# Kernel optimization log

Measured on AMD Instinct MI355X. Metric: run time of the kernel, lower is better.

Reference implementation:

```python
import jax, jax.numpy as jnp
import numpy as np

PC_RANGE = (-51.2, -51.2, -5.0, 51.2, 51.2, 3.0)
IMG_H, IMG_W = 256.0, 704.0
EPS = 1e-5


def conv2d(x, w, b, pad):
    y = jax.lax.conv_general_dilated(x, w, (1, 1), ((pad, pad), (pad, pad)),
                                     dimension_numbers=('NCHW', 'OIHW', 'NCHW'))
    return y + b[None, :, None, None]


def bilinear_sample(feat, grid):
    # torch.F.grid_sample, bilinear, zeros padding, align_corners=False
    # feat (BN,C,H,W), grid (BN,Q,D,2) in [-1,1] -> (BN,C,Q,D)
    BN, C, H, W = feat.shape
    ix = (grid[..., 0] + 1.0) * (W * 0.5) - 0.5
    iy = (grid[..., 1] + 1.0) * (H * 0.5) - 0.5
    x0 = jnp.floor(ix); y0 = jnp.floor(iy)
    x1 = x0 + 1.0; y1 = y0 + 1.0
    wx1 = ix - x0; wx0 = 1.0 - wx1
    wy1 = iy - y0; wy0 = 1.0 - wy1

    def corner(f, xi, yi):
        inb = ((xi >= 0) & (xi < W) & (yi >= 0) & (yi < H)).astype(f.dtype)
        xc = jnp.clip(xi, 0, W - 1).astype(jnp.int32)
        yc = jnp.clip(yi, 0, H - 1).astype(jnp.int32)
        idx = (yc * W + xc).reshape(-1)
        v = f.reshape(C, H * W)[:, idx].reshape((C,) + xi.shape)
        return v * inb[None]

    def sample_one(f, x0b, y0b, x1b, y1b, w00, w01, w10, w11):
        return (corner(f, x0b, y0b) * w00[None] + corner(f, x1b, y0b) * w01[None]
                + corner(f, x0b, y1b) * w10[None] + corner(f, x1b, y1b) * w11[None])

    return jax.vmap(sample_one)(feat, x0, y0, x1, y1,
                                wx0 * wy0, wx1 * wy0, wx0 * wy1, wx1 * wy1)


def ihr_forward(feat, bev_queries, bev_pos, reference_points, lidar2img, img_aug,
                w_pos, b_pos, w_attn, b_attn, w_out, b_out,
                conv_w, conv_b, bn_gamma, bn_beta, bn_mean, bn_var,
                se_w, se_b, cbam_w, cbam_b, bev_h, bev_w):
    B, Q, C = bev_queries.shape
    N = lidar2img.shape[1]
    q = bev_queries + bev_pos
    off = q @ w_pos + b_pos                                   # (B,Q,1) height offset
    # only_use_height: z <- sigmoid(inverse_sigmoid(z) + off)
    z = jnp.clip(reference_points[..., 2:3], 0.0, 1.0)
    z = jnp.log(jnp.clip(z, EPS, None) / jnp.clip(1.0 - z, EPS, None))
    z = jax.nn.sigmoid(z + off[:, None])                      # (B,D,Q,1)
    rp = jnp.concatenate([reference_points[..., :2], z], -1)  # updated ref points

    # --- feature_sampling ---
    xyz = jnp.stack([
        rp[..., 0] * (PC_RANGE[3] - PC_RANGE[0]) + PC_RANGE[0],
        rp[..., 1] * (PC_RANGE[4] - PC_RANGE[1]) + PC_RANGE[1],
        rp[..., 2] * (PC_RANGE[5] - PC_RANGE[2]) + PC_RANGE[2]], -1)  # (B,D,Q,3)
    pts = jnp.concatenate([xyz, jnp.ones_like(xyz[..., :1])], -1)
    pts = jnp.transpose(pts, (1, 0, 2, 3))                    # (D,B,Q,4)
    D = pts.shape[0]
    cam = jnp.einsum('bnij,dbqj->dbnqi', lidar2img, pts)       # (D,B,N,Q,3)
    depth = cam[..., 2:3]
    mask = depth > EPS
    cam4 = jnp.concatenate([cam[..., :2] / jnp.maximum(depth, EPS), depth,
                            jnp.ones_like(depth)], -1)
    cam2 = jnp.einsum('bnij,dbnqj->dbnqi', img_aug, cam4)[..., :2]
    cam2 = cam2 / jnp.array([IMG_W, IMG_H], cam2.dtype)
    cam2 = (cam2 - 0.5) * 2.0
    mask = (mask & (cam2[..., 0:1] > -1.0) & (cam2[..., 0:1] < 1.0)
            & (cam2[..., 1:2] > -1.0) & (cam2[..., 1:2] < 1.0))
    bev_mask = jnp.nan_to_num(jnp.transpose(mask, (1, 4, 3, 2, 0)).astype(feat.dtype))  # (B,1,Q,N,D)
    grid = jnp.transpose(cam2, (1, 2, 3, 0, 4)).reshape(B * N, Q, D, 2)
    samp = bilinear_sample(feat, grid)                         # (BN,C,Q,D)
    samp = samp.reshape(B, N, C, Q, D).transpose(0, 2, 3, 1, 4)  # (B,C,Q,N,D)
    samp = jnp.nan_to_num(samp)

    attn = jax.nn.sigmoid(q @ w_attn + b_attn).reshape(B, 1, Q, N, 1) * bev_mask
    out = (samp * attn).sum(axis=(3, 4))                       # (B,C,Q)  (D==1)
    out = out.transpose(0, 2, 1) @ w_out + b_out + bev_queries  # (B,Q,C)

    # --- vtransform: Conv3x3 -> BN(eval) -> ReLU -> SE -> CBAM(spatial) ---
    x = out.transpose(0, 2, 1).reshape(B, C, bev_h, bev_w)
    x = conv2d(x, conv_w, conv_b, 1)
    inv = jax.lax.rsqrt(bn_var + 1e-5)
    x = bn_gamma[None, :, None, None] * (x - bn_mean[None, :, None, None]) * inv[None, :, None, None] + bn_beta[None, :, None, None]
    x = jax.nn.relu(x)
    s = jax.nn.sigmoid(x.mean(axis=(2, 3)) @ se_w + se_b)      # SE: GAP + 1x1 conv
    x = x * s[:, :, None, None]
    mx = x.max(axis=1, keepdims=True)
    av = x.mean(axis=1, keepdims=True)
    a = jax.nn.sigmoid(conv2d(jnp.concatenate([mx, av], 1), cbam_w, cbam_b, 3))
    x = x * a
    out = x.reshape(B, C, bev_h * bev_w).transpose(0, 2, 1)
    return out, rp


def setup_inputs() -> dict:
    key = jax.random.key(0)
    ks = jax.random.split(key, 16)
    B, N, C, Q, D = 1, 6, 256, 128 * 128, 1
    H, W = 32, 88
    return {
        'feat': jax.random.normal(ks[0], (B * N, C, H, W), jnp.float32),
        'bev_queries': jax.random.normal(ks[1], (B, Q, C), jnp.float32),
        'bev_pos': jax.random.normal(ks[2], (B, Q, C), jnp.float32),
        'reference_points': jax.random.uniform(ks[3], (B, D, Q, 3), jnp.float32),
        'lidar2img': jax.random.normal(ks[4], (B, N, 3, 4), jnp.float32),
        'img_aug': jax.random.normal(ks[5], (B, N, 3, 4), jnp.float32),
        'w_pos': jax.random.normal(ks[6], (C, 1), jnp.float32) * 0.02,
        'b_pos': jnp.zeros((1,), jnp.float32),
        'w_attn': jax.random.normal(ks[7], (C, N), jnp.float32) * 0.02,
        'b_attn': jnp.zeros((N,), jnp.float32),
        'w_out': jax.random.normal(ks[8], (C, C), jnp.float32) * 0.02,
        'b_out': jnp.zeros((C,), jnp.float32),
        'conv_w': jax.random.normal(ks[9], (C, C, 3, 3), jnp.float32) * 0.02,
        'conv_b': jnp.zeros((C,), jnp.float32),
        'bn_gamma': jnp.ones((C,), jnp.float32),
        'bn_beta': jnp.zeros((C,), jnp.float32),
        'bn_mean': jnp.zeros((C,), jnp.float32),
        'bn_var': jax.random.uniform(ks[10], (C,), jnp.float32, 0.5, 1.5),
        'se_w': jax.random.normal(ks[11], (C, C), jnp.float32) * 0.02,
        'se_b': jnp.zeros((C,), jnp.float32),
        'cbam_w': jax.random.normal(ks[12], (1, 2, 7, 7), jnp.float32) * 0.1,
        'cbam_b': jnp.zeros((1,), jnp.float32),
        'bev_h': 128,
        'bev_w': 128,
    }


def reference(feat, bev_queries, bev_pos, reference_points, lidar2img, img_aug,
              w_pos, b_pos, w_attn, b_attn, w_out, b_out,
              conv_w, conv_b, bn_gamma, bn_beta, bn_mean, bn_var,
              se_w, se_b, cbam_w, cbam_b, bev_h, bev_w):
    return ihr_forward(feat, bev_queries, bev_pos, reference_points, lidar2img, img_aug,
                       w_pos, b_pos, w_attn, b_attn, w_out, b_out,
                       conv_w, conv_b, bn_gamma, bn_beta, bn_mean, bn_var,
                       se_w, se_b, cbam_w, cbam_b, bev_h, bev_w)
```

## Files before the change

kernel.cpp:

```cpp
#include <hip/hip_runtime.h>

typedef float  f32x4 __attribute__((ext_vector_type(4)));
typedef short  s16x8 __attribute__((ext_vector_type(8)));
typedef short  s16x4 __attribute__((ext_vector_type(4)));

__device__ __forceinline__ float bf2f(short h) {
    union { unsigned u; float f; } v; v.u = ((unsigned)(unsigned short)h) << 16; return v.f;
}
__device__ __forceinline__ short f2bf(float f) {
    union { float f; unsigned u; } v; v.f = f;
    unsigned r = v.u + 0x7FFFu + ((v.u >> 16) & 1u);
    return (short)(r >> 16);
}
__device__ __forceinline__ float sigf(float x) { return 1.f / (1.f + __expf(-x)); }

__device__ __forceinline__ void gll16(const void* g, void* l) {
    __builtin_amdgcn_global_load_lds(
        (const __attribute__((address_space(1))) unsigned int*)(uintptr_t)g,
        (__attribute__((address_space(3))) unsigned int*)(uintptr_t)l,
        16, 0, 0);
}


__global__ __launch_bounds__(256) void k_prep(
    const float* __restrict__ feat, const float* __restrict__ w_out,
    const float* __restrict__ conv_w, short* __restrict__ featT,
    short* __restrict__ woT, short* __restrict__ w9,
    short* __restrict__ Xp, float* __restrict__ chan_sums)
{
    __shared__ float tile[64][65];
    int b = blockIdx.x, t = threadIdx.x;
    if (b < 2340) {
        ((f32x4*)Xp)[b * 256 + t] = (f32x4){0.f, 0.f, 0.f, 0.f};
    } else if (b < 3396) {
        int bb = b - 2340;
        int n = bb / 176, r = bb % 176, ct = r / 44, ht = r % 44;
        int ty = t >> 6, tx = t & 63;
        const float* src = feat + (n * 256 + ct * 64) * 2816 + ht * 64;
        #pragma unroll
        for (int i = 0; i < 16; ++i) {
            int cl = ty * 16 + i;
            tile[cl][tx] = src[cl * 2816 + tx];
        }
        __syncthreads();
        short* dst = featT + (n * 2816 + ht * 64) * 256 + ct * 64;
        #pragma unroll
        for (int i = 0; i < 16; ++i) {
            int row = ty * 16 + i;
            dst[row * 256 + tx] = f2bf(tile[tx][row]);
        }
    } else if (b < 3652) {
        int idx = (b - 3396) * 256 + t;
        int j = idx >> 8, c = idx & 255;
        woT[j * 256 + c] = f2bf(w_out[c * 256 + j]);
    } else if (b < 3908) {
        int oc = (b - 3652) * 256 + t;
        const float* src = conv_w + oc * 9;
        #pragma unroll
        for (int k = 0; k < 9; ++k) w9[k * 65536 + oc] = f2bf(src[k]);
    } else {
        if (t < 256) chan_sums[t] = 0.f;
    }
}

__global__ __launch_bounds__(256) void k_sample(
    const float* __restrict__ bev_q, const float* __restrict__ bev_pos,
    const float* __restrict__ refp, const float* __restrict__ l2i,
    const float* __restrict__ aug, const float* __restrict__ w_pos,
    const float* __restrict__ b_pos, const float* __restrict__ w_attn,
    const float* __restrict__ b_attn, const short* __restrict__ featT,
    short* __restrict__ S, float* __restrict__ rp_out)
{
    int lane = threadIdx.x & 63;
    int qi = blockIdx.x * 4 + (threadIdx.x >> 6);

    f32x4 qv = *(const f32x4*)(bev_q + qi * 256 + lane * 4);
    {
        f32x4 pv = *(const f32x4*)(bev_pos + qi * 256 + lane * 4);
        qv[0] += pv[0]; qv[1] += pv[1]; qv[2] += pv[2]; qv[3] += pv[3];
    }
    f32x4 wp = *(const f32x4*)(w_pos + lane * 4);
    float op = qv[0]*wp[0] + qv[1]*wp[1] + qv[2]*wp[2] + qv[3]*wp[3];

    float la[6] = {0.f,0.f,0.f,0.f,0.f,0.f};
    const float* wa = w_attn + lane * 24;
    #pragma unroll
    for (int i = 0; i < 4; ++i) {
        #pragma unroll
        for (int n = 0; n < 6; ++n) la[n] += qv[i] * wa[i * 6 + n];
    }
    #pragma unroll
    for (int m = 1; m < 64; m <<= 1) {
        op += __shfl_xor(op, m);
        #pragma unroll
        for (int n = 0; n < 6; ++n) la[n] += __shfl_xor(la[n], m);
    }
    float off = op + b_pos[0];
    float attn[6];
    #pragma unroll
    for (int n = 0; n < 6; ++n) attn[n] = sigf(la[n] + b_attn[n]);

    float rx = refp[qi * 3 + 0], ry = refp[qi * 3 + 1], rz = refp[qi * 3 + 2];
    float zc = fminf(fmaxf(rz, 0.f), 1.f);
    float lg = logf(fmaxf(zc, 1e-5f) / fmaxf(1.f - zc, 1e-5f));
    float zn = sigf(lg + off);
    if (lane == 0) {
        rp_out[qi * 3 + 0] = rx;
        rp_out[qi * 3 + 1] = ry;
        rp_out[qi * 3 + 2] = zn;
    }

    float X = rx * 102.4f - 51.2f;
    float Yc = ry * 102.4f - 51.2f;
    float Z = zn * 8.f - 5.f;

    f32x4 acc = {0.f, 0.f, 0.f, 0.f};
    auto corner = [&](int n, int xi, int yi, float w) {
        if (xi >= 0 && xi < 88 && yi >= 0 && yi < 32) {
            s16x4 v = *(const s16x4*)(featT + (((n * 32 + yi) * 88 + xi) << 8) + (lane << 2));
            acc[0] += w * bf2f(v[0]); acc[1] += w * bf2f(v[1]);
            acc[2] += w * bf2f(v[2]); acc[3] += w * bf2f(v[3]);
        }
    };
    for (int n = 0; n < 6; ++n) {
        const float* L = l2i + n * 12;
        float cx = L[0]*X + L[1]*Yc + L[2]*Z  + L[3];
        float cy = L[4]*X + L[5]*Yc + L[6]*Z  + L[7];
        float d  = L[8]*X + L[9]*Yc + L[10]*Z + L[11];
        float dd = fmaxf(d, 1e-5f);
        float ux = cx / dd, uy = cy / dd;
        const float* A = aug + n * 12;
        float ax = A[0]*ux + A[1]*uy + A[2]*d + A[3];
        float ay = A[4]*ux + A[5]*uy + A[6]*d + A[7];
        float gx = (ax * (1.f / 704.f) - 0.5f) * 2.f;
        float gy = (ay * (1.f / 256.f) - 0.5f) * 2.f;
        bool m = (d > 1e-5f) && (gx > -1.f) && (gx < 1.f) && (gy > -1.f) && (gy < 1.f);
        if (m) {
            float ix = (gx + 1.f) * 44.f - 0.5f;
            float iy = (gy + 1.f) * 16.f - 0.5f;
            float x0f = floorf(ix), y0f = floorf(iy);
            float wx1 = ix - x0f, wx0 = 1.f - wx1;
            float wy1 = iy - y0f, wy0 = 1.f - wy1;
            int x0 = (int)x0f, y0 = (int)y0f, x1 = x0 + 1, y1 = y0 + 1;
            float wn = attn[n];
            corner(n, x0, y0, wn * wx0 * wy0);
            corner(n, x1, y0, wn * wx1 * wy0);
            corner(n, x0, y1, wn * wx0 * wy1);
            corner(n, x1, y1, wn * wx1 * wy1);
        }
    }
    s16x4 sv;
    sv[0] = f2bf(acc[0]); sv[1] = f2bf(acc[1]);
    sv[2] = f2bf(acc[2]); sv[3] = f2bf(acc[3]);
    *(s16x4*)(S + qi * 256 + lane * 4) = sv;
}

__global__ __launch_bounds__(256) void k_gemm(
    const short* __restrict__ S, const short* __restrict__ woT,
    const float* __restrict__ b_out, const float* __restrict__ bev_q,
    short* __restrict__ Xp)
{
    int tid = threadIdx.x, wave = tid >> 6, lane = tid & 63;
    int l15 = lane & 15, quad = lane >> 4;
    int p0 = blockIdx.x * 64, n0 = wave * 64;
    f32x4 acc[4][4];
    #pragma unroll
    for (int mt = 0; mt < 4; ++mt)
        #pragma unroll
        for (int nt = 0; nt < 4; ++nt) acc[mt][nt] = (f32x4){0.f,0.f,0.f,0.f};

    const short* Ab = S   + (p0 + l15) * 256 + quad * 8;
    const short* Bb = woT + (n0 + l15) * 256 + quad * 8;
    #pragma unroll
    for (int kb = 0; kb < 8; ++kb) {
        s16x8 a[4], b[4];
        #pragma unroll
        for (int mt = 0; mt < 4; ++mt) a[mt] = *(const s16x8*)(Ab + mt * 4096 + kb * 32);
        #pragma unroll
        for (int nt = 0; nt < 4; ++nt) b[nt] = *(const s16x8*)(Bb + nt * 4096 + kb * 32);
        #pragma unroll
        for (int mt = 0; mt < 4; ++mt)
            #pragma unroll
            for (int nt = 0; nt < 4; ++nt)
                acc[mt][nt] = __builtin_amdgcn_mfma_f32_16x16x32_bf16(a[mt], b[nt], acc[mt][nt], 0, 0, 0);
    }
    #pragma unroll
    for (int nt = 0; nt < 4; ++nt) {
        int j = n0 + nt * 16 + l15;
        float bo = b_out[j];
        #pragma unroll
        for (int mt = 0; mt < 4; ++mt) {
            #pragma unroll
            for (int r = 0; r < 4; ++r) {
                int p = p0 + mt * 16 + quad * 4 + r;
                float v = acc[mt][nt][r] + bo + bev_q[p * 256 + j];
                int h = p >> 7, w = p & 127;
                Xp[((h + 1) * 144 + (w + 1)) * 256 + j] = f2bf(v);
            }
        }
    }
}

__global__ __launch_bounds__(256) void k_conv(
    const short* __restrict__ Xp, const short* __restrict__ w9,
    const float* __restrict__ conv_b, const float* __restrict__ gamma,
    const float* __restrict__ beta, const float* __restrict__ mean,
    const float* __restrict__ var, short* __restrict__ Y)
{
    __shared__ short lds[32768];

    int tid = threadIdx.x, wave = tid >> 6, lane = tid & 63;
    int l15 = lane & 15, quad = lane >> 4;
    int sg = lane >> 3, cg = lane & 7;
    int cgx = cg ^ sg;
    int b = blockIdx.x;
    int och = (b >> 3) & 1;
    int h = (b & 7) * 16 + (b >> 4);
    int mi = wave & 1, ni = wave >> 1;

    f32x4 acc[4][4];
    #pragma unroll
    for (int mt = 0; mt < 4; ++mt)
        #pragma unroll
        for (int nt = 0; nt < 4; ++nt) acc[mt][nt] = (f32x4){0.f,0.f,0.f,0.f};

    auto stage = [&](int t) {
        int tap = t >> 2, cb = t & 3;
        int kh = tap / 3, kw = tap % 3;
        int c0 = cb << 6;
        const short* wsrc = w9 + (tap << 16) + (och << 15) + c0 + cgx * 8;
        const short* xsrc = Xp + ((h + kh) * 144 + kw) * 256 + c0 + cgx * 8;
        short* la = &lds[(t & 1) << 14];
        short* lb = la + 8192;
        #pragma unroll
        for (int j = 0; j < 4; ++j) {
            int row = j * 32 + wave * 8 + sg;
            int slot = (j * 256 + wave * 64 + lane) * 8;
            gll16(wsrc + row * 256, &la[slot]);
            gll16(xsrc + row * 256, &lb[slot]);
        }
    };

    stage(0);
    for (int t = 0; t < 36; ++t) {
        asm volatile("s_waitcnt vmcnt(0)\n\ts_barrier" ::: "memory");
        if (t < 35) stage(t + 1);
        const short* la = &lds[(t & 1) << 14];
        const short* lb = la + 8192;
        int rsw = l15 & 7;
        #pragma unroll
        for (int s = 0; s < 2; ++s) {
            int cgk = s * 4 + quad;
            int csw = (cgk ^ rsw) * 8;
            s16x8 af[4], bf[4];
            #pragma unroll
            for (int mt = 0; mt < 4; ++mt)
                af[mt] = *(const s16x8*)&la[(mi * 64 + mt * 16 + l15) * 64 + csw];
            #pragma unroll
            for (int nt = 0; nt < 4; ++nt)
                bf[nt] = *(const s16x8*)&lb[(ni * 64 + nt * 16 + l15) * 64 + csw];
            #pragma unroll
            for (int mt = 0; mt < 4; ++mt)
                #pragma unroll
                for (int nt = 0; nt < 4; ++nt)
                    acc[mt][nt] = __builtin_amdgcn_mfma_f32_16x16x32_bf16(af[mt], bf[nt], acc[mt][nt], 0, 0, 0);
        }
    }

    #pragma unroll
    for (int mt = 0; mt < 4; ++mt) {
        #pragma unroll
        for (int r = 0; r < 4; ++r) {
            int o = (och << 7) + mi * 64 + mt * 16 + quad * 4 + r;
            float cb_ = conv_b[o], g = gamma[o], be = beta[o], mu = mean[o];
            float inv = rsqrtf(var[o] + 1e-5f);
            #pragma unroll
            for (int nt = 0; nt < 4; ++nt) {
                int p = h * 128 + ni * 64 + nt * 16 + l15;
                float v = acc[mt][nt][r] + cb_;
                v = g * (v - mu) * inv + be;
                Y[p * 256 + o] = f2bf(fmaxf(v, 0.f));
            }
        }
    }
}

__global__ __launch_bounds__(256) void k_csum(const short* __restrict__ Y, float* __restrict__ chan_sums)
{
    int c = threadIdx.x, p0 = blockIdx.x * 64;
    float s = 0.f;
    for (int i = 0; i < 64; ++i) s += bf2f(Y[(p0 + i) * 256 + c]);
    atomicAdd(chan_sums + c, s);
}

__global__ __launch_bounds__(256) void k_se(
    const float* __restrict__ chan_sums, const float* __restrict__ se_w,
    const float* __restrict__ se_b, float* __restrict__ sbuf)
{
    __shared__ float m[256];
    int t = threadIdx.x;
    m[t] = chan_sums[t] * (1.f / 16384.f);
    __syncthreads();
    float a = 0.f;
    for (int c = 0; c < 256; ++c) a += m[c] * se_w[c * 256 + t];
    sbuf[t] = sigf(a + se_b[t]);
}

__global__ __launch_bounds__(256) void k_mxav(
    const short* __restrict__ Y, const float* __restrict__ sbuf,
    float* __restrict__ mx, float* __restrict__ av)
{
    int lane = threadIdx.x & 63;
    int p = blockIdx.x * 4 + (threadIdx.x >> 6);
    f32x4 sv = *(const f32x4*)(sbuf + lane * 4);
    s16x4 yv = *(const s16x4*)(Y + p * 256 + lane * 4);
    float v0 = bf2f(yv[0]) * sv[0], v1 = bf2f(yv[1]) * sv[1];
    float v2 = bf2f(yv[2]) * sv[2], v3 = bf2f(yv[3]) * sv[3];
    float mval = fmaxf(fmaxf(v0, v1), fmaxf(v2, v3));
    float aval = v0 + v1 + v2 + v3;
    #pragma unroll
    for (int m = 1; m < 64; m <<= 1) {
        mval = fmaxf(mval, __shfl_xor(mval, m));
        aval += __shfl_xor(aval, m);
    }
    if (lane == 0) { mx[p] = mval; av[p] = aval * (1.f / 256.f); }
}

__global__ __launch_bounds__(256) void k_cbam(
    const float* __restrict__ mx, const float* __restrict__ av,
    const float* __restrict__ cw, const float* __restrict__ cb,
    float* __restrict__ amap)
{
    int p = blockIdx.x * 256 + threadIdx.x;
    int h = p >> 7, w = p & 127;
    float acc = cb[0];
    for (int kh = 0; kh < 7; ++kh) {
        int yy = h + kh - 3;
        if ((unsigned)yy >= 128u) continue;
        for (int kw = 0; kw < 7; ++kw) {
            int xx = w + kw - 3;
            if ((unsigned)xx >= 128u) continue;
            int q = yy * 128 + xx;
            acc += cw[kh * 7 + kw] * mx[q] + cw[49 + kh * 7 + kw] * av[q];
        }
    }
    amap[p] = sigf(acc);
}

__global__ __launch_bounds__(256) void k_final(
    const short* __restrict__ Y, const float* __restrict__ sbuf,
    const float* __restrict__ amap, float* __restrict__ out0)
{
    int lane = threadIdx.x & 63;
    int p = blockIdx.x * 4 + (threadIdx.x >> 6);
    float a = amap[p];
    f32x4 sv = *(const f32x4*)(sbuf + lane * 4);
    s16x4 yv = *(const s16x4*)(Y + p * 256 + lane * 4);
    f32x4 o;
    o[0] = bf2f(yv[0]) * sv[0] * a;
    o[1] = bf2f(yv[1]) * sv[1] * a;
    o[2] = bf2f(yv[2]) * sv[2] * a;
    o[3] = bf2f(yv[3]) * sv[3] * a;
    *(f32x4*)(out0 + p * 256 + lane * 4) = o;
}

extern "C" void kernel_launch(void* const* d_in, const int* in_sizes, int n_in,
                              void* d_out, int out_size, void* d_ws, size_t ws_size,
                              hipStream_t stream) {
    const float* feat     = (const float*)d_in[0];
    const float* bev_q    = (const float*)d_in[1];
    const float* bev_pos  = (const float*)d_in[2];
    const float* refp     = (const float*)d_in[3];
    const float* l2i      = (const float*)d_in[4];
    const float* aug      = (const float*)d_in[5];
    const float* w_pos    = (const float*)d_in[6];
    const float* b_pos    = (const float*)d_in[7];
    const float* w_attn   = (const float*)d_in[8];
    const float* b_attn   = (const float*)d_in[9];
    const float* w_out    = (const float*)d_in[10];
    const float* b_out    = (const float*)d_in[11];
    const float* conv_w   = (const float*)d_in[12];
    const float* conv_b   = (const float*)d_in[13];
    const float* bn_g     = (const float*)d_in[14];
    const float* bn_b     = (const float*)d_in[15];
    const float* bn_m     = (const float*)d_in[16];
    const float* bn_v     = (const float*)d_in[17];
    const float* se_w     = (const float*)d_in[18];
    const float* se_b     = (const float*)d_in[19];
    const float* cbam_w   = (const float*)d_in[20];
    const float* cbam_b   = (const float*)d_in[21];

    char* ws = (char*)d_ws;
    short* featT     = (short*)(ws + 0);
    short* Ybuf      = (short*)(ws + 0);
    short* Sbuf      = (short*)(ws + 8650752);
    short* Xp        = (short*)(ws + 17039360);
    short* w9        = (short*)(ws + 26624000);
    short* woT       = (short*)(ws + 27803648);
    float* chan_sums = (float*)(ws + 27934720);
    float* sbuf      = (float*)(ws + 27935744);
    float* mx        = (float*)(ws + 27936768);
    float* av        = (float*)(ws + 28002304);
    float* amap      = (float*)(ws + 28067840);

    float* out0   = (float*)d_out;
    float* rp_out = out0 + 16384 * 256;

    hipLaunchKernelGGL(k_prep, dim3(3909), dim3(256), 0, stream,
                       feat, w_out, conv_w, featT, woT, w9, Xp, chan_sums);
    hipLaunchKernelGGL(k_sample, dim3(4096), dim3(256), 0, stream,
                       bev_q, bev_pos, refp, l2i, aug, w_pos, b_pos, w_attn, b_attn,
                       featT, Sbuf, rp_out);
    hipLaunchKernelGGL(k_gemm, dim3(256), dim3(256), 0, stream,
                       Sbuf, woT, b_out, bev_q, Xp);
    hipLaunchKernelGGL(k_conv, dim3(256), dim3(256), 0, stream,
                       Xp, w9, conv_b, bn_g, bn_b, bn_m, bn_v, Ybuf);
    hipLaunchKernelGGL(k_csum, dim3(256), dim3(256), 0, stream, Ybuf, chan_sums);
    hipLaunchKernelGGL(k_se, dim3(1), dim3(256), 0, stream, chan_sums, se_w, se_b, sbuf);
    hipLaunchKernelGGL(k_mxav, dim3(4096), dim3(256), 0, stream, Ybuf, sbuf, mx, av);
    hipLaunchKernelGGL(k_cbam, dim3(64), dim3(256), 0, stream, mx, av, cbam_w, cbam_b, amap);
    hipLaunchKernelGGL(k_final, dim3(4096), dim3(256), 0, stream, Ybuf, sbuf, amap, out0);
}
```

Before: 239.2 us.

## Fuse sampling into GEMM, channel sums into conv, and merge tail kernels

The bilinear sampling now writes its bf16 rows into a swizzled LDS tile, and the output-projection GEMM in the same block reads that tile, so the S buffer never goes through global memory. Channel sums for SE are computed in the conv epilogue with shuffles and atomics, which removes the separate column-sum pass. The SE, max/avg, CBAM and final-scale kernels collapse into two tail kernels that each recompute the SE gate per block. In exchange, sampling now runs on only 256 blocks of 16 rows per wave, which lowers parallelism for the gather-heavy phase, and the SE matvec is repeated 512 times.

After: 292.6 us. 22.3% more time.

```diff
diff --git a/kernel.cpp b/kernel.cpp
--- a/kernel.cpp
+++ b/kernel.cpp
@@ -63,119 +63,125 @@
     }
 }
 
-__global__ __launch_bounds__(256) void k_sample(
+__global__ __launch_bounds__(256) void k_sampgemm(
     const float* __restrict__ bev_q, const float* __restrict__ bev_pos,
     const float* __restrict__ refp, const float* __restrict__ l2i,
     const float* __restrict__ aug, const float* __restrict__ w_pos,
     const float* __restrict__ b_pos, const float* __restrict__ w_attn,
     const float* __restrict__ b_attn, const short* __restrict__ featT,
-    short* __restrict__ S, float* __restrict__ rp_out)
+    const short* __restrict__ woT, const float* __restrict__ b_out,
+    short* __restrict__ Xp, float* __restrict__ rp_out)
 {
-    int lane = threadIdx.x & 63;
-    int qi = blockIdx.x * 4 + (threadIdx.x >> 6);
-
-    f32x4 qv = *(const f32x4*)(bev_q + qi * 256 + lane * 4);
-    {
-        f32x4 pv = *(const f32x4*)(bev_pos + qi * 256 + lane * 4);
-        qv[0] += pv[0]; qv[1] += pv[1]; qv[2] += pv[2]; qv[3] += pv[3];
-    }
-    f32x4 wp = *(const f32x4*)(w_pos + lane * 4);
-    float op = qv[0]*wp[0] + qv[1]*wp[1] + qv[2]*wp[2] + qv[3]*wp[3];
-
-    float la[6] = {0.f,0.f,0.f,0.f,0.f,0.f};
-    const float* wa = w_attn + lane * 24;
-    #pragma unroll
-    for (int i = 0; i < 4; ++i) {
-        #pragma unroll
-        for (int n = 0; n < 6; ++n) la[n] += qv[i] * wa[i * 6 + n];
-    }
-    #pragma unroll
-    for (int m = 1; m < 64; m <<= 1) {
-        op += __shfl_xor(op, m);
-        #pragma unroll
-        for (int n = 0; n < 6; ++n) la[n] += __shfl_xor(la[n], m);
-    }
-    float off = op + b_pos[0];
-    float attn[6];
-    #pragma unroll
-    for (int n = 0; n < 6; ++n) attn[n] = sigf(la[n] + b_attn[n]);
-
-    float rx = refp[qi * 3 + 0], ry = refp[qi * 3 + 1], rz = refp[qi * 3 + 2];
-    float zc = fminf(fmaxf(rz, 0.f), 1.f);
-    float lg = logf(fmaxf(zc, 1e-5f) / fmaxf(1.f - zc, 1e-5f));
-    float zn = sigf(lg + off);
-    if (lane == 0) {
-        rp_out[qi * 3 + 0] = rx;
-        rp_out[qi * 3 + 1] = ry;
-        rp_out[qi * 3 + 2] = zn;
-    }
-
-    float X = rx * 102.4f - 51.2f;
-    float Yc = ry * 102.4f - 51.2f;
-    float Z = zn * 8.f - 5.f;
-
-    f32x4 acc = {0.f, 0.f, 0.f, 0.f};
-    auto corner = [&](int n, int xi, int yi, float w) {
-        if (xi >= 0 && xi < 88 && yi >= 0 && yi < 32) {
-            s16x4 v = *(const s16x4*)(featT + (((n * 32 + yi) * 88 + xi) << 8) + (lane << 2));
-            acc[0] += w * bf2f(v[0]); acc[1] += w * bf2f(v[1]);
-            acc[2] += w * bf2f(v[2]); acc[3] += w * bf2f(v[3]);
-        }
-    };
-    for (int n = 0; n < 6; ++n) {
-        const float* L = l2i + n * 12;
-        float cx = L[0]*X + L[1]*Yc + L[2]*Z  + L[3];
-        float cy = L[4]*X + L[5]*Yc + L[6]*Z  + L[7];
-        float d  = L[8]*X + L[9]*Yc + L[10]*Z + L[11];
-        float dd = fmaxf(d, 1e-5f);
-        float ux = cx / dd, uy = cy / dd;
-        const float* A = aug + n * 12;
-        float ax = A[0]*ux + A[1]*uy + A[2]*d + A[3];
-        float ay = A[4]*ux + A[5]*uy + A[6]*d + A[7];
-        float gx = (ax * (1.f / 704.f) - 0.5f) * 2.f;
-        float gy = (ay * (1.f / 256.f) - 0.5f) * 2.f;
-        bool m = (d > 1e-5f) && (gx > -1.f) && (gx < 1.f) && (gy > -1.f) && (gy < 1.f);
-        if (m) {
-            float ix = (gx + 1.f) * 44.f - 0.5f;
-            float iy = (gy + 1.f) * 16.f - 0.5f;
-            float x0f = floorf(ix), y0f = floorf(iy);
-            float wx1 = ix - x0f, wx0 = 1.f - wx1;
-            float wy1 = iy - y0f, wy0 = 1.f - wy1;
-            int x0 = (int)x0f, y0 = (int)y0f, x1 = x0 + 1, y1 = y0 + 1;
-            float wn = attn[n];
-            corner(n, x0, y0, wn * wx0 * wy0);
-            corner(n, x1, y0, wn * wx1 * wy0);
-            corner(n, x0, y1, wn * wx0 * wy1);
-            corner(n, x1, y1, wn * wx1 * wy1);
-        }
-    }
-    s16x4 sv;
-    sv[0] = f2bf(acc[0]); sv[1] = f2bf(acc[1]);
-    sv[2] = f2bf(acc[2]); sv[3] = f2bf(acc[3]);
-    *(s16x4*)(S + qi * 256 + lane * 4) = sv;
-}
-
-__global__ __launch_bounds__(256) void k_gemm(
-    const short* __restrict__ S, const short* __restrict__ woT,
-    const float* __restrict__ b_out, const float* __restrict__ bev_q,
-    short* __restrict__ Xp)
-{
+    __shared__ short lS[64 * 256];
+
     int tid = threadIdx.x, wave = tid >> 6, lane = tid & 63;
+    int p0 = blockIdx.x * 64;
+
+    for (int i = 0; i < 16; ++i) {
+        int r = wave * 16 + i;
+        int qi = p0 + r;
+
+        f32x4 qv = *(const f32x4*)(bev_q + qi * 256 + lane * 4);
+        {
+            f32x4 pv = *(const f32x4*)(bev_pos + qi * 256 + lane * 4);
+            qv[0] += pv[0]; qv[1] += pv[1]; qv[2] += pv[2]; qv[3] += pv[3];
+        }
+        f32x4 wp = *(const f32x4*)(w_pos + lane * 4);
+        float op = qv[0]*wp[0] + qv[1]*wp[1] + qv[2]*wp[2] + qv[3]*wp[3];
+
+        float la[6] = {0.f,0.f,0.f,0.f,0.f,0.f};
+        const float* wa = w_attn + lane * 24;
+        #pragma unroll
+        for (int ii = 0; ii < 4; ++ii) {
+            #pragma unroll
+            for (int n = 0; n < 6; ++n) la[n] += qv[ii] * wa[ii * 6 + n];
+        }
+        #pragma unroll
+        for (int m = 1; m < 64; m <<= 1) {
+            op += __shfl_xor(op, m);
+            #pragma unroll
+            for (int n = 0; n < 6; ++n) la[n] += __shfl_xor(la[n], m);
+        }
+        float off = op + b_pos[0];
+        float attn[6];
+        #pragma unroll
+        for (int n = 0; n < 6; ++n) attn[n] = sigf(la[n] + b_attn[n]);
+
+        float rx = refp[qi * 3 + 0], ry = refp[qi * 3 + 1], rz = refp[qi * 3 + 2];
+        float zc = fminf(fmaxf(rz, 0.f), 1.f);
+        float lg = logf(fmaxf(zc, 1e-5f) / fmaxf(1.f - zc, 1e-5f));
+        float zn = sigf(lg + off);
+        if (lane == 0) {
+            rp_out[qi * 3 + 0] = rx;
+            rp_out[qi * 3 + 1] = ry;
+            rp_out[qi * 3 + 2] = zn;
+        }
+
+        float X = rx * 102.4f - 51.2f;
+        float Yc = ry * 102.4f - 51.2f;
+        float Z = zn * 8.f - 5.f;
+
+        f32x4 acc = {0.f, 0.f, 0.f, 0.f};
+        auto corner = [&](int n, int xi, int yi, float w) {
+            if (xi >= 0 && xi < 88 && yi >= 0 && yi < 32) {
+                s16x4 v = *(const s16x4*)(featT + (((n * 32 + yi) * 88 + xi) << 8) + (lane << 2));
+                acc[0] += w * bf2f(v[0]); acc[1] += w * bf2f(v[1]);
+                acc[2] += w * bf2f(v[2]); acc[3] += w * bf2f(v[3]);
+            }
+        };
+        for (int n = 0; n < 6; ++n) {
+            const float* L = l2i + n * 12;
+            float cx = L[0]*X + L[1]*Yc + L[2]*Z  + L[3];
+            float cy = L[4]*X + L[5]*Yc + L[6]*Z  + L[7];
+            float d  = L[8]*X + L[9]*Yc + L[10]*Z + L[11];
+            float dd = fmaxf(d, 1e-5f);
+            float ux = cx / dd, uy = cy / dd;
+            const float* A = aug + n * 12;
+            float ax = A[0]*ux + A[1]*uy + A[2]*d + A[3];
+            float ay = A[4]*ux + A[5]*uy + A[6]*d + A[7];
+            float gx = (ax * (1.f / 704.f) - 0.5f) * 2.f;
+            float gy = (ay * (1.f / 256.f) - 0.5f) * 2.f;
+            bool m = (d > 1e-5f) && (gx > -1.f) && (gx < 1.f) && (gy > -1.f) && (gy < 1.f);
+            if (m) {
+                float ix = (gx + 1.f) * 44.f - 0.5f;
+                float iy = (gy + 1.f) * 16.f - 0.5f;
+                float x0f = floorf(ix), y0f = floorf(iy);
+                float wx1 = ix - x0f, wx0 = 1.f - wx1;
+                float wy1 = iy - y0f, wy0 = 1.f - wy1;
+                int x0 = (int)x0f, y0 = (int)y0f, x1 = x0 + 1, y1 = y0 + 1;
+                float wn = attn[n];
+                corner(n, x0, y0, wn * wx0 * wy0);
+                corner(n, x1, y0, wn * wx1 * wy0);
+                corner(n, x0, y1, wn * wx0 * wy1);
+                corner(n, x1, y1, wn * wx1 * wy1);
+            }
+        }
+        s16x4 sv;
+        sv[0] = f2bf(acc[0]); sv[1] = f2bf(acc[1]);
+        sv[2] = f2bf(acc[2]); sv[3] = f2bf(acc[3]);
+        int g = lane >> 1, hf = lane & 1;
+        *(s16x4*)&lS[(r * 32 + (g ^ (r & 7))) * 8 + hf * 4] = sv;
+    }
+    __syncthreads();
+
     int l15 = lane & 15, quad = lane >> 4;
-    int p0 = blockIdx.x * 64, n0 = wave * 64;
+    int n0 = wave * 64;
     f32x4 acc[4][4];
     #pragma unroll
     for (int mt = 0; mt < 4; ++mt)
         #pragma unroll
         for (int nt = 0; nt < 4; ++nt) acc[mt][nt] = (f32x4){0.f,0.f,0.f,0.f};
 
-    const short* Ab = S   + (p0 + l15) * 256 + quad * 8;
     const short* Bb = woT + (n0 + l15) * 256 + quad * 8;
     #pragma unroll
     for (int kb = 0; kb < 8; ++kb) {
         s16x8 a[4], b[4];
         #pragma unroll
-        for (int mt = 0; mt < 4; ++mt) a[mt] = *(const s16x8*)(Ab + mt * 4096 + kb * 32);
+        for (int mt = 0; mt < 4; ++mt) {
+            int row = mt * 16 + l15;
+            int pg = (quad + kb * 4) ^ (row & 7);
+            a[mt] = *(const s16x8*)&lS[(row * 32 + pg) * 8];
+        }
         #pragma unroll
         for (int nt = 0; nt < 4; ++nt) b[nt] = *(const s16x8*)(Bb + nt * 4096 + kb * 32);
         #pragma unroll
@@ -205,7 +211,8 @@
     const short* __restrict__ Xp, const short* __restrict__ w9,
     const float* __restrict__ conv_b, const float* __restrict__ gamma,
     const float* __restrict__ beta, const float* __restrict__ mean,
-    const float* __restrict__ var, short* __restrict__ Y)
+    const float* __restrict__ var, short* __restrict__ Y,
+    float* __restrict__ chan_sums)
 {
     __shared__ short lds[32768];
 
@@ -274,94 +281,113 @@
             int o = (och << 7) + mi * 64 + mt * 16 + quad * 4 + r;
             float cb_ = conv_b[o], g = gamma[o], be = beta[o], mu = mean[o];
             float inv = rsqrtf(var[o] + 1e-5f);
+            float s = 0.f;
             #pragma unroll
             for (int nt = 0; nt < 4; ++nt) {
                 int p = h * 128 + ni * 64 + nt * 16 + l15;
                 float v = acc[mt][nt][r] + cb_;
                 v = g * (v - mu) * inv + be;
-                Y[p * 256 + o] = f2bf(fmaxf(v, 0.f));
+                v = fmaxf(v, 0.f);
+                Y[p * 256 + o] = f2bf(v);
+                s += v;
             }
-        }
-    }
-}
-
-__global__ __launch_bounds__(256) void k_csum(const short* __restrict__ Y, float* __restrict__ chan_sums)
-{
-    int c = threadIdx.x, p0 = blockIdx.x * 64;
-    float s = 0.f;
-    for (int i = 0; i < 64; ++i) s += bf2f(Y[(p0 + i) * 256 + c]);
-    atomicAdd(chan_sums + c, s);
-}
-
-__global__ __launch_bounds__(256) void k_se(
+            s += __shfl_xor(s, 1);
+            s += __shfl_xor(s, 2);
+            s += __shfl_xor(s, 4);
+            s += __shfl_xor(s, 8);
+            if (l15 == 0) atomicAdd(chan_sums + o, s);
+        }
+    }
+}
+
+__global__ __launch_bounds__(256) void k_tail1(
     const float* __restrict__ chan_sums, const float* __restrict__ se_w,
-    const float* __restrict__ se_b, float* __restrict__ sbuf)
-{
-    __shared__ float m[256];
-    int t = threadIdx.x;
-    m[t] = chan_sums[t] * (1.f / 16384.f);
-    __syncthreads();
-    float a = 0.f;
-    for (int c = 0; c < 256; ++c) a += m[c] * se_w[c * 256 + t];
-    sbuf[t] = sigf(a + se_b[t]);
-}
-
-__global__ __launch_bounds__(256) void k_mxav(
-    const short* __restrict__ Y, const float* __restrict__ sbuf,
+    const float* __restrict__ se_b, const short* __restrict__ Y,
     float* __restrict__ mx, float* __restrict__ av)
 {
-    int lane = threadIdx.x & 63;
-    int p = blockIdx.x * 4 + (threadIdx.x >> 6);
-    f32x4 sv = *(const f32x4*)(sbuf + lane * 4);
-    s16x4 yv = *(const s16x4*)(Y + p * 256 + lane * 4);
-    float v0 = bf2f(yv[0]) * sv[0], v1 = bf2f(yv[1]) * sv[1];
-    float v2 = bf2f(yv[2]) * sv[2], v3 = bf2f(yv[3]) * sv[3];
-    float mval = fmaxf(fmaxf(v0, v1), fmaxf(v2, v3));
-    float aval = v0 + v1 + v2 + v3;
-    #pragma unroll
-    for (int m = 1; m < 64; m <<= 1) {
-        mval = fmaxf(mval, __shfl_xor(mval, m));
-        aval += __shfl_xor(aval, m);
-    }
-    if (lane == 0) { mx[p] = mval; av[p] = aval * (1.f / 256.f); }
-}
-
-__global__ __launch_bounds__(256) void k_cbam(
-    const float* __restrict__ mx, const float* __restrict__ av,
-    const float* __restrict__ cw, const float* __restrict__ cb,
-    float* __restrict__ amap)
+    __shared__ float sm[256];
+    __shared__ float smx[256];
+    int t = threadIdx.x;
+    sm[t] = chan_sums[t] * (1.f / 16384.f);
+    __syncthreads();
+    {
+        float a = 0.f;
+        for (int c = 0; c < 256; ++c) a += sm[c] * se_w[c * 256 + t];
+        smx[t] = sigf(a + se_b[t]);
+    }
+    __syncthreads();
+
+    int lane = t & 63, wv = t >> 6;
+    f32x4 sv = *(const f32x4*)&smx[lane * 4];
+    for (int i = 0; i < 16; ++i) {
+        int p = blockIdx.x * 64 + i * 4 + wv;
+        s16x4 yv = *(const s16x4*)(Y + p * 256 + lane * 4);
+        float v0 = bf2f(yv[0]) * sv[0], v1 = bf2f(yv[1]) * sv[1];
+        float v2 = bf2f(yv[2]) * sv[2], v3 = bf2f(yv[3]) * sv[3];
+        float mval = fmaxf(fmaxf(v0, v1), fmaxf(v2, v3));
+        float aval = v0 + v1 + v2 + v3;
+        #pragma unroll
+        for (int m = 1; m < 64; m <<= 1) {
+            mval = fmaxf(mval, __shfl_xor(mval, m));
+            aval += __shfl_xor(aval, m);
+        }
+        if (lane == 0) { mx[p] = mval; av[p] = aval * (1.f / 256.f); }
+    }
+}
+
+__global__ __launch_bounds__(256) void k_tail2(
+    const float* __restrict__ chan_sums, const float* __restrict__ se_w,
+    const float* __restrict__ se_b, const float* __restrict__ mx,
+    const float* __restrict__ av, const float* __restrict__ cw,
+    const float* __restrict__ cb, const short* __restrict__ Y,
+    float* __restrict__ out0)
 {
-    int p = blockIdx.x * 256 + threadIdx.x;
-    int h = p >> 7, w = p & 127;
-    float acc = cb[0];
-    for (int kh = 0; kh < 7; ++kh) {
-        int yy = h + kh - 3;
-        if ((unsigned)yy >= 128u) continue;
-        for (int kw = 0; kw < 7; ++kw) {
-            int xx = w + kw - 3;
-            if ((unsigned)xx >= 128u) continue;
-            int q = yy * 128 + xx;
-            acc += cw[kh * 7 + kw] * mx[q] + cw[49 + kh * 7 + kw] * av[q];
-        }
-    }
-    amap[p] = sigf(acc);
-}
-
-__global__ __launch_bounds__(256) void k_final(
-    const short* __restrict__ Y, const float* __restrict__ sbuf,
-    const float* __restrict__ amap, float* __restrict__ out0)
-{
-    int lane = threadIdx.x & 63;
-    int p = blockIdx.x * 4 + (threadIdx.x >> 6);
-    float a = amap[p];
-    f32x4 sv = *(const f32x4*)(sbuf + lane * 4);
-    s16x4 yv = *(const s16x4*)(Y + p * 256 + lane * 4);
-    f32x4 o;
-    o[0] = bf2f(yv[0]) * sv[0] * a;
-    o[1] = bf2f(yv[1]) * sv[1] * a;
-    o[2] = bf2f(yv[2]) * sv[2] * a;
-    o[3] = bf2f(yv[3]) * sv[3] * a;
-    *(f32x4*)(out0 + p * 256 + lane * 4) = o;
+    __shared__ float sm[256];
+    __shared__ float smx[256];
+    __shared__ float samap[64];
+    int t = threadIdx.x;
+    sm[t] = chan_sums[t] * (1.f / 16384.f);
+    __syncthreads();
+    {
+        float a = 0.f;
+        for (int c = 0; c < 256; ++c) a += sm[c] * se_w[c * 256 + t];
+        smx[t] = sigf(a + se_b[t]);
+    }
+    __syncthreads();
+
+    int p0 = blockIdx.x * 64;
+    if (t < 64) {
+        int p = p0 + t;
+        int h = p >> 7, w = p & 127;
+        float acc = cb[0];
+        for (int kh = 0; kh < 7; ++kh) {
+            int yy = h + kh - 3;
+            if ((unsigned)yy >= 128u) continue;
+            for (int kw = 0; kw < 7; ++kw) {
+                int xx = w + kw - 3;
+                if ((unsigned)xx >= 128u) continue;
+                int q = yy * 128 + xx;
+                acc += cw[kh * 7 + kw] * mx[q] + cw[49 + kh * 7 + kw] * av[q];
+            }
+        }
+        samap[t] = sigf(acc);
+    }
+    __syncthreads();
+
+    int lane = t & 63, wv = t >> 6;
+    f32x4 sv = *(const f32x4*)&smx[lane * 4];
+    for (int i = 0; i < 16; ++i) {
+        int r = i * 4 + wv;
+        int p = p0 + r;
+        float a = samap[r];
+        s16x4 yv = *(const s16x4*)(Y + p * 256 + lane * 4);
+        f32x4 o;
+        o[0] = bf2f(yv[0]) * sv[0] * a;
+        o[1] = bf2f(yv[1]) * sv[1] * a;
+        o[2] = bf2f(yv[2]) * sv[2] * a;
+        o[3] = bf2f(yv[3]) * sv[3] * a;
+        *(f32x4*)(out0 + p * 256 + lane * 4) = o;
+    }
 }
 
 extern "C" void kernel_launch(void* const* d_in, const int* in_sizes, int n_in,
@@ -393,31 +419,25 @@
     char* ws = (char*)d_ws;
     short* featT     = (short*)(ws + 0);
     short* Ybuf      = (short*)(ws + 0);
-    short* Sbuf      = (short*)(ws + 8650752);
     short* Xp        = (short*)(ws + 17039360);
     short* w9        = (short*)(ws + 26624000);
     short* woT       = (short*)(ws + 27803648);
     float* chan_sums = (float*)(ws + 27934720);
-    float* sbuf      = (float*)(ws + 27935744);
     float* mx        = (float*)(ws + 27936768);
     float* av        = (float*)(ws + 28002304);
-    float* amap      = (float*)(ws + 28067840);
 
     float* out0   = (float*)d_out;
     float* rp_out = out0 + 16384 * 256;
 
     hipLaunchKernelGGL(k_prep, dim3(3909), dim3(256), 0, stream,
                        feat, w_out, conv_w, featT, woT, w9, Xp, chan_sums);
-    hipLaunchKernelGGL(k_sample, dim3(4096), dim3(256), 0, stream,
+    hipLaunchKernelGGL(k_sampgemm, dim3(256), dim3(256), 0, stream,
                        bev_q, bev_pos, refp, l2i, aug, w_pos, b_pos, w_attn, b_attn,
-                       featT, Sbuf, rp_out);
-    hipLaunchKernelGGL(k_gemm, dim3(256), dim3(256), 0, stream,
-                       Sbuf, woT, b_out, bev_q, Xp);
+                       featT, woT, b_out, Xp, rp_out);
     hipLaunchKernelGGL(k_conv, dim3(256), dim3(256), 0, stream,
-                       Xp, w9, conv_b, bn_g, bn_b, bn_m, bn_v, Ybuf);
-    hipLaunchKernelGGL(k_csum, dim3(256), dim3(256), 0, stream, Ybuf, chan_sums);
-    hipLaunchKernelGGL(k_se, dim3(1), dim3(256), 0, stream, chan_sums, se_w, se_b, sbuf);
-    hipLaunchKernelGGL(k_mxav, dim3(4096), dim3(256), 0, stream, Ybuf, sbuf, mx, av);
-    hipLaunchKernelGGL(k_cbam, dim3(64), dim3(256), 0, stream, mx, av, cbam_w, cbam_b, amap);
-    hipLaunchKernelGGL(k_final, dim3(4096), dim3(256), 0, stream, Ybuf, sbuf, amap, out0);
-}
+                       Xp, w9, conv_b, bn_g, bn_b, bn_m, bn_v, Ybuf, chan_sums);
+    hipLaunchKernelGGL(k_tail1, dim3(256), dim3(256), 0, stream,
+                       chan_sums, se_w, se_b, Ybuf, mx, av);
+    hipLaunchKernelGGL(k_tail2, dim3(256), dim3(256), 0, stream,
+                       chan_sums, se_w, se_b, mx, av, cbam_w, cbam_b, Ybuf, out0);
+}
```

## Load conv weights directly into registers from fragment-ordered layout, halve conv tile

Applied to the files above, without the earlier changes.

The prep kernel now writes the 3x3 conv weights in an MFMA-fragment-friendly layout, so the conv kernel loads A fragments straight from global memory into double-buffered registers instead of staging them through LDS. The conv tile shrinks from 128 output pixels to 64 (half a row), doubling the grid to 512 blocks, and LDS use drops to the activation buffer only. This aims to cut LDS traffic and improve occupancy and load balance across CUs, at the cost of more registers for prefetched weights, redundant weight reads across blocks, and less reuse of each weight fragment.

New measurement: 243.5 us. About the same (+1.8%).

```diff
diff --git a/kernel.cpp b/kernel.cpp
--- a/kernel.cpp
+++ b/kernel.cpp
@@ -25,7 +25,7 @@
 __global__ __launch_bounds__(256) void k_prep(
     const float* __restrict__ feat, const float* __restrict__ w_out,
     const float* __restrict__ conv_w, short* __restrict__ featT,
-    short* __restrict__ woT, short* __restrict__ w9,
+    short* __restrict__ woT, short* __restrict__ w9f,
     short* __restrict__ Xp, float* __restrict__ chan_sums)
 {
     __shared__ float tile[64][65];
@@ -55,9 +55,12 @@
         woT[j * 256 + c] = f2bf(w_out[c * 256 + j]);
     } else if (b < 3908) {
         int oc = (b - 3652) * 256 + t;
+        int o = oc >> 8, c = oc & 255;
         const float* src = conv_w + oc * 9;
-        #pragma unroll
-        for (int k = 0; k < 9; ++k) w9[k * 65536 + oc] = f2bf(src[k]);
+        int base = (o >> 4) * 32 * 128 + (c >> 3) * 128 + (o & 15) * 8 + (c & 7);
+        #pragma unroll
+        for (int k = 0; k < 9; ++k)
+            w9f[k * 65536 + base] = f2bf(src[k]);
     } else {
         if (t < 256) chan_sums[t] = 0.f;
     }
@@ -202,68 +205,76 @@
 }
 
 __global__ __launch_bounds__(256) void k_conv(
-    const short* __restrict__ Xp, const short* __restrict__ w9,
+    const short* __restrict__ Xp, const short* __restrict__ w9f,
     const float* __restrict__ conv_b, const float* __restrict__ gamma,
     const float* __restrict__ beta, const float* __restrict__ mean,
     const float* __restrict__ var, short* __restrict__ Y)
 {
-    __shared__ short lds[32768];
+    __shared__ short lB[8192];
 
     int tid = threadIdx.x, wave = tid >> 6, lane = tid & 63;
     int l15 = lane & 15, quad = lane >> 4;
     int sg = lane >> 3, cg = lane & 7;
     int cgx = cg ^ sg;
     int b = blockIdx.x;
-    int och = (b >> 3) & 1;
-    int h = (b & 7) * 16 + (b >> 4);
-    int mi = wave & 1, ni = wave >> 1;
-
-    f32x4 acc[4][4];
+    int xcd = b & 7, bi = b >> 3;
+    int och = bi >> 5, lp = bi & 31;
+    int h = xcd * 16 + (lp >> 1);
+    int w0 = (lp & 1) * 64;
+    int mi = wave >> 1, ni = wave & 1;
+
+    f32x4 acc[4][2];
     #pragma unroll
     for (int mt = 0; mt < 4; ++mt)
         #pragma unroll
-        for (int nt = 0; nt < 4; ++nt) acc[mt][nt] = (f32x4){0.f,0.f,0.f,0.f};
-
-    auto stage = [&](int t) {
+        for (int nt = 0; nt < 2; ++nt) acc[mt][nt] = (f32x4){0.f,0.f,0.f,0.f};
+
+    s16x8 afr[2][8];
+
+    const short* w9base = w9f + ((och * 8 + mi * 4) * 32 + quad) * 128 + l15 * 8;
+    auto loadA = [&](int t, int par) {
+        int tap = t >> 2, cb = t & 3;
+        const short* base = w9base + tap * 65536 + cb * 8 * 128;
+        #pragma unroll
+        for (int s = 0; s < 2; ++s)
+            #pragma unroll
+            for (int mt = 0; mt < 4; ++mt)
+                afr[par][s * 4 + mt] = *(const s16x8*)(base + (mt * 32 + s * 4) * 128);
+    };
+    auto stageB = [&](int t) {
         int tap = t >> 2, cb = t & 3;
         int kh = tap / 3, kw = tap % 3;
-        int c0 = cb << 6;
-        const short* wsrc = w9 + (tap << 16) + (och << 15) + c0 + cgx * 8;
-        const short* xsrc = Xp + ((h + kh) * 144 + kw) * 256 + c0 + cgx * 8;
-        short* la = &lds[(t & 1) << 14];
-        short* lb = la + 8192;
-        #pragma unroll
-        for (int j = 0; j < 4; ++j) {
-            int row = j * 32 + wave * 8 + sg;
-            int slot = (j * 256 + wave * 64 + lane) * 8;
-            gll16(wsrc + row * 256, &la[slot]);
-            gll16(xsrc + row * 256, &lb[slot]);
+        const short* xsrc = Xp + ((h + kh) * 144 + (w0 + kw)) * 256 + cb * 64 + cgx * 8;
+        short* lb = &lB[(t & 1) << 12];
+        #pragma unroll
+        for (int j = 0; j < 2; ++j) {
+            int px = j * 32 + (tid >> 3);
+            gll16(xsrc + px * 256, &lb[(j * 256 + tid) * 8]);
         }
     };
 
-    stage(0);
+    loadA(0, 0);
+    stageB(0);
+    #pragma unroll
     for (int t = 0; t < 36; ++t) {
         asm volatile("s_waitcnt vmcnt(0)\n\ts_barrier" ::: "memory");
-        if (t < 35) stage(t + 1);
-        const short* la = &lds[(t & 1) << 14];
-        const short* lb = la + 8192;
+        if (t < 35) { loadA(t + 1, (t + 1) & 1); stageB(t + 1); }
+        const short* lb = &lB[(t & 1) << 12];
         int rsw = l15 & 7;
         #pragma unroll
         for (int s = 0; s < 2; ++s) {
             int cgk = s * 4 + quad;
             int csw = (cgk ^ rsw) * 8;
-            s16x8 af[4], bf[4];
-            #pragma unroll
-            for (int mt = 0; mt < 4; ++mt)
-                af[mt] = *(const s16x8*)&la[(mi * 64 + mt * 16 + l15) * 64 + csw];
-            #pragma unroll
-            for (int nt = 0; nt < 4; ++nt)
-                bf[nt] = *(const s16x8*)&lb[(ni * 64 + nt * 16 + l15) * 64 + csw];
+            s16x8 bf[2];
+            #pragma unroll
+            for (int nt = 0; nt < 2; ++nt)
+                bf[nt] = *(const s16x8*)&lb[(ni * 32 + nt * 16 + l15) * 64 + csw];
             #pragma unroll
             for (int mt = 0; mt < 4; ++mt)
                 #pragma unroll
-                for (int nt = 0; nt < 4; ++nt)
-                    acc[mt][nt] = __builtin_amdgcn_mfma_f32_16x16x32_bf16(af[mt], bf[nt], acc[mt][nt], 0, 0, 0);
+                for (int nt = 0; nt < 2; ++nt)
+                    acc[mt][nt] = __builtin_amdgcn_mfma_f32_16x16x32_bf16(
+                        afr[t & 1][s * 4 + mt], bf[nt], acc[mt][nt], 0, 0, 0);
         }
     }
 
@@ -271,12 +282,12 @@
     for (int mt = 0; mt < 4; ++mt) {
         #pragma unroll
         for (int r = 0; r < 4; ++r) {
-            int o = (och << 7) + mi * 64 + mt * 16 + quad * 4 + r;
+            int o = och * 128 + mi * 64 + mt * 16 + quad * 4 + r;
             float cb_ = conv_b[o], g = gamma[o], be = beta[o], mu = mean[o];
             float inv = rsqrtf(var[o] + 1e-5f);
             #pragma unroll
-            for (int nt = 0; nt < 4; ++nt) {
-                int p = h * 128 + ni * 64 + nt * 16 + l15;
+            for (int nt = 0; nt < 2; ++nt) {
+                int p = h * 128 + w0 + ni * 32 + nt * 16 + l15;
                 float v = acc[mt][nt][r] + cb_;
                 v = g * (v - mu) * inv + be;
                 Y[p * 256 + o] = f2bf(fmaxf(v, 0.f));
@@ -395,7 +406,7 @@
     short* Ybuf      = (short*)(ws + 0);
     short* Sbuf      = (short*)(ws + 8650752);
     short* Xp        = (short*)(ws + 17039360);
-    short* w9        = (short*)(ws + 26624000);
+    short* w9f       = (short*)(ws + 26624000);
     short* woT       = (short*)(ws + 27803648);
     float* chan_sums = (float*)(ws + 27934720);
     float* sbuf      = (float*)(ws + 27935744);
@@ -407,14 +418,14 @@
     float* rp_out = out0 + 16384 * 256;
 
     hipLaunchKernelGGL(k_prep, dim3(3909), dim3(256), 0, stream,
-                       feat, w_out, conv_w, featT, woT, w9, Xp, chan_sums);
+                       feat, w_out, conv_w, featT, woT, w9f, Xp, chan_sums);
     hipLaunchKernelGGL(k_sample, dim3(4096), dim3(256), 0, stream,
                        bev_q, bev_pos, refp, l2i, aug, w_pos, b_pos, w_attn, b_attn,
                        featT, Sbuf, rp_out);
     hipLaunchKernelGGL(k_gemm, dim3(256), dim3(256), 0, stream,
                        Sbuf, woT, b_out, bev_q, Xp);
-    hipLaunchKernelGGL(k_conv, dim3(256), dim3(256), 0, stream,
-                       Xp, w9, conv_b, bn_g, bn_b, bn_m, bn_v, Ybuf);
+    hipLaunchKernelGGL(k_conv, dim3(512), dim3(256), 0, stream,
+                       Xp, w9f, conv_b, bn_g, bn_b, bn_m, bn_v, Ybuf);
     hipLaunchKernelGGL(k_csum, dim3(256), dim3(256), 0, stream, Ybuf, chan_sums);
     hipLaunchKernelGGL(k_se, dim3(1), dim3(256), 0, stream, chan_sums, se_w, se_b, sbuf);
     hipLaunchKernelGGL(k_mxav, dim3(4096), dim3(256), 0, stream, Ybuf, sbuf, mx, av);
```

## Triple-buffer conv LDS pipeline, remap blocks per XCD, parallelize SE matvec

Applied to the files above, without the earlier changes.

The 3x3 conv kernel moves from double to triple buffering in LDS with prefetch distance two, waiting only on older loads (vmcnt(8)) so global-to-LDS copies overlap more MFMA work. The block-to-(row, output-half) mapping is changed so each XCD works on a contiguous band of rows, which should improve L2 reuse of the padded input. The SE matvec is split across 8 blocks, with 8 threads per output channel reducing partial sums, instead of one block doing the whole product serially. Raising LDS use to 96KB per block may limit how many blocks fit on a CU.

After: 223.4 us, median of 2. 1.07x faster.

```diff
diff --git a/kernel.cpp b/kernel.cpp
--- a/kernel.cpp
+++ b/kernel.cpp
@@ -207,15 +207,16 @@
     const float* __restrict__ beta, const float* __restrict__ mean,
     const float* __restrict__ var, short* __restrict__ Y)
 {
-    __shared__ short lds[32768];
+    __shared__ short lds[49152];
 
     int tid = threadIdx.x, wave = tid >> 6, lane = tid & 63;
     int l15 = lane & 15, quad = lane >> 4;
     int sg = lane >> 3, cg = lane & 7;
     int cgx = cg ^ sg;
     int b = blockIdx.x;
-    int och = (b >> 3) & 1;
-    int h = (b & 7) * 16 + (b >> 4);
+    int xcd = b & 7, bi = b >> 3;
+    int och = bi >> 4;
+    int h = xcd * 16 + (bi & 15);
     int mi = wave & 1, ni = wave >> 1;
 
     f32x4 acc[4][4];
@@ -230,7 +231,7 @@
         int c0 = cb << 6;
         const short* wsrc = w9 + (tap << 16) + (och << 15) + c0 + cgx * 8;
         const short* xsrc = Xp + ((h + kh) * 144 + kw) * 256 + c0 + cgx * 8;
-        short* la = &lds[(t & 1) << 14];
+        short* la = &lds[(t % 3) * 16384];
         short* lb = la + 8192;
         #pragma unroll
         for (int j = 0; j < 4; ++j) {
@@ -242,10 +243,13 @@
     };
 
     stage(0);
+    stage(1);
+    #pragma unroll
     for (int t = 0; t < 36; ++t) {
-        asm volatile("s_waitcnt vmcnt(0)\n\ts_barrier" ::: "memory");
-        if (t < 35) stage(t + 1);
-        const short* la = &lds[(t & 1) << 14];
+        if (t < 35) asm volatile("s_waitcnt vmcnt(8)\n\ts_barrier" ::: "memory");
+        else        asm volatile("s_waitcnt vmcnt(0)\n\ts_barrier" ::: "memory");
+        if (t < 34) stage(t + 2);
+        const short* la = &lds[(t % 3) * 16384];
         const short* lb = la + 8192;
         int rsw = l15 & 7;
         #pragma unroll
@@ -298,12 +302,25 @@
     const float* __restrict__ se_b, float* __restrict__ sbuf)
 {
     __shared__ float m[256];
+    __shared__ float part[256];
     int t = threadIdx.x;
     m[t] = chan_sums[t] * (1.f / 16384.f);
     __syncthreads();
+    int j = blockIdx.x * 32 + (t >> 3);
+    int cseg = t & 7;
     float a = 0.f;
-    for (int c = 0; c < 256; ++c) a += m[c] * se_w[c * 256 + t];
-    sbuf[t] = sigf(a + se_b[t]);
+    #pragma unroll
+    for (int i = 0; i < 32; ++i) {
+        int c = cseg * 32 + i;
+        a += m[c] * se_w[c * 256 + j];
+    }
+    part[t] = a;
+    __syncthreads();
+    if (cseg == 0) {
+        float s = part[t] + part[t+1] + part[t+2] + part[t+3]
+                + part[t+4] + part[t+5] + part[t+6] + part[t+7];
+        sbuf[j] = sigf(s + se_b[j]);
+    }
 }
 
 __global__ __launch_bounds__(256) void k_mxav(
@@ -416,7 +433,7 @@
     hipLaunchKernelGGL(k_conv, dim3(256), dim3(256), 0, stream,
                        Xp, w9, conv_b, bn_g, bn_b, bn_m, bn_v, Ybuf);
     hipLaunchKernelGGL(k_csum, dim3(256), dim3(256), 0, stream, Ybuf, chan_sums);
-    hipLaunchKernelGGL(k_se, dim3(1), dim3(256), 0, stream, chan_sums, se_w, se_b, sbuf);
+    hipLaunchKernelGGL(k_se, dim3(8), dim3(256), 0, stream, chan_sums, se_w, se_b, sbuf);
     hipLaunchKernelGGL(k_mxav, dim3(4096), dim3(256), 0, stream, Ybuf, sbuf, mx, av);
     hipLaunchKernelGGL(k_cbam, dim3(64), dim3(256), 0, stream, mx, av, cbam_w, cbam_b, amap);
     hipLaunchKernelGGL(k_final, dim3(4096), dim3(256), 0, stream, Ybuf, sbuf, amap, out0);
```
